# Performance work log

Hardware: AMD Instinct MI355X
Metric: run time of the kernel (lower is better)

## Reference

```python
import jax, jax.numpy as jnp
import numpy as np

HEAD_DIM = 128
N_HEADS = 16
N_KV_HEADS = 4
CHUNK = 256
TOPK = 4
ROPE_THETA = 10000.0


def apply_rope(x, pos):
    # x: [B, S, H, D], NeoX-style (half-split) rotary as in flash-attn RotaryEmbedding
    d = x.shape[-1]
    inv_freq = 1.0 / (ROPE_THETA ** (jnp.arange(0, d, 2, dtype=jnp.float32) / d))  # [D/2]
    ang = pos.astype(jnp.float32)[:, None] * inv_freq[None, :]  # [S, D/2]
    cos = jnp.cos(ang)[None, :, None, :]
    sin = jnp.sin(ang)[None, :, None, :]
    x1, x2 = x[..., : d // 2], x[..., d // 2:]
    return jnp.concatenate([x1 * cos - x2 * sin, x2 * cos + x1 * sin], axis=-1)


def setup_inputs() -> dict:
    key = jax.random.key(0)
    ks = jax.random.split(key, 5)
    B, S, H = 2, 2048, 2048
    hidden_states = jax.random.normal(ks[0], (B, S, H), dtype=jnp.float32)
    wq = jax.random.normal(ks[1], (H, N_HEADS * HEAD_DIM), dtype=jnp.float32) * 0.02
    wk = jax.random.normal(ks[2], (H, N_KV_HEADS * HEAD_DIM), dtype=jnp.float32) * 0.02
    wv = jax.random.normal(ks[3], (H, N_KV_HEADS * HEAD_DIM), dtype=jnp.float32) * 0.02
    wo = jax.random.normal(ks[4], (N_HEADS * HEAD_DIM, H), dtype=jnp.float32) * 0.02
    return {"hidden_states": hidden_states, "wq": wq, "wk": wk, "wv": wv, "wo": wo}


def reference(hidden_states, wq, wk, wv, wo):
    B, S, _ = hidden_states.shape
    q = (hidden_states @ wq).reshape(B, S, N_HEADS, HEAD_DIM)
    k = (hidden_states @ wk).reshape(B, S, N_KV_HEADS, HEAD_DIM)
    v = (hidden_states @ wv).reshape(B, S, N_KV_HEADS, HEAD_DIM)

    pos = jnp.arange(S)
    q = apply_rope(q, pos)
    k = apply_rope(k, pos)

    # GQA: repeat_interleave kv heads to match query heads
    g = N_HEADS // N_KV_HEADS
    k = jnp.repeat(k, g, axis=2)  # [B,S,H,D]
    v = jnp.repeat(v, g, axis=2)

    # ---- MoBA gating: q . mean(K_chunk) ----
    N = S // CHUNK  # number of chunks
    kmean = k.reshape(B, N, CHUNK, N_HEADS, HEAD_DIM).mean(axis=2)  # [B,N,H,D]
    gate = jnp.einsum('bnhd,bshd->bhsn', kmean, q)  # [B,H,S,N]

    chunk_ids = jnp.arange(N)
    chunk_end = (chunk_ids + 1) * CHUNK
    q_chunk = pos // CHUNK
    # chunks not fully before the query are not gate candidates
    gate = jnp.where(pos[None, None, :, None] >= chunk_end[None, None, None, :], gate, -jnp.inf)
    # query's own chunk is always selected
    gate = jnp.where(q_chunk[None, None, :, None] == chunk_ids[None, None, None, :], jnp.inf, gate)

    _, idx = jax.lax.top_k(gate, min(TOPK, N))  # [B,H,S,K]
    sel = jnp.any(idx[..., None] == chunk_ids, axis=-2)  # [B,H,S,N] bool

    # expand chunk selection to per-key mask; combine with causal mask
    allowed = sel[:, :, :, pos // CHUNK]  # [B,H,S,S]
    causal = pos[:, None] >= pos[None, :]  # [S,S]
    mask = allowed & causal[None, None]

    scale = HEAD_DIM ** -0.5
    scores = jnp.einsum('bshd,bthd->bhst', q, k) * scale
    scores = jnp.where(mask, scores, -jnp.inf)
    probs = jax.nn.softmax(scores, axis=-1)
    o = jnp.einsum('bhst,bthd->bshd', probs, v).reshape(B, S, N_HEADS * HEAD_DIM)
    return o @ wo
```

## Files before the change

kernel.cpp:

```cpp
#include <hip/hip_runtime.h>
#include <stdint.h>
#include <math.h>

typedef _Float16 f16x8 __attribute__((ext_vector_type(8)));
typedef float    f32x4 __attribute__((ext_vector_type(4)));
typedef __attribute__((address_space(1))) void as1_void;
typedef __attribute__((address_space(3))) void as3_void;

__device__ __forceinline__ unsigned short f2h(float x) {
    _Float16 h = (_Float16)x;
    return __builtin_bit_cast(unsigned short, h);
}
__device__ __forceinline__ float h2f(unsigned short u) {
    return (float)__builtin_bit_cast(_Float16, u);
}
__device__ __forceinline__ void glds16(const void* g, void* l) {
    __builtin_amdgcn_global_load_lds((as1_void*)g, (as3_void*)l, 16, 0, 0);
}


#define TAU 0.015

__global__ void setup_kernel(float* __restrict__ ct, float* __restrict__ st,
                             double* __restrict__ km, int* __restrict__ flagcnt) {
    int gid = blockIdx.x * 256 + threadIdx.x;
    if (gid == 0) *flagcnt = 0;
    if (gid < 8192) km[gid] = 0.0;
    int i = gid & 63, s = gid >> 6;
    float xf = (float)i * (1.0f / 64.0f);
    float pf = (float)pow(10000.0, (double)xf);
    float inv = 1.0f / pf;
    float ang = (float)s * inv;
    ct[gid] = (float)cos((double)ang);
    st[gid] = (float)sin((double)ang);
}

__global__ __launch_bounds__(256)
void ksum_kernel(const float* __restrict__ hs, const float* __restrict__ ct,
                 const float* __restrict__ st, double* __restrict__ Act,
                 double* __restrict__ Ast) {
    __shared__ float Hs[16][68];
    __shared__ float Tc[16][68];
    __shared__ float Ts[16][68];
    int bn = blockIdx.y;
    int h0 = blockIdx.x * 64;
    int b = bn >> 3, n = bn & 7;
    int t = threadIdx.x;
    int tx = t & 15, ty = t >> 4;
    int d0 = tx * 4, hl0 = ty * 4;
    int si = t & 15, g4 = (t >> 4) * 4;
    double ac[4][4] = {}, as_[4][4] = {};
    for (int s0 = 0; s0 < 256; s0 += 16) {
        __syncthreads();
        int srow = n * 256 + s0 + si;
        *(float4*)&Hs[si][g4] = *(const float4*)&hs[(size_t)(b * 2048 + srow) * 2048 + h0 + g4];
        *(float4*)&Tc[si][g4] = *(const float4*)&ct[srow * 64 + g4];
        *(float4*)&Ts[si][g4] = *(const float4*)&st[srow * 64 + g4];
        __syncthreads();
        #pragma unroll
        for (int kk = 0; kk < 16; ++kk) {
            double hv[4], cv[4], sv[4];
            #pragma unroll
            for (int j = 0; j < 4; ++j) hv[j] = (double)Hs[kk][hl0 + j];
            #pragma unroll
            for (int i = 0; i < 4; ++i) { cv[i] = (double)Tc[kk][d0 + i]; sv[i] = (double)Ts[kk][d0 + i]; }
            #pragma unroll
            for (int i = 0; i < 4; ++i)
                #pragma unroll
                for (int j = 0; j < 4; ++j) {
                    ac[i][j]  = fma(cv[i], hv[j], ac[i][j]);
                    as_[i][j] = fma(sv[i], hv[j], as_[i][j]);
                }
        }
    }
    #pragma unroll
    for (int j = 0; j < 4; ++j) {
        size_t rb = ((size_t)bn * 2048 + h0 + hl0 + j) * 64 + d0;
        double2 c0 = {ac[0][j], ac[1][j]},  c1 = {ac[2][j], ac[3][j]};
        double2 s0_ = {as_[0][j], as_[1][j]}, s1_ = {as_[2][j], as_[3][j]};
        *(double2*)&Act[rb] = c0; *(double2*)&Act[rb + 2] = c1;
        *(double2*)&Ast[rb] = s0_; *(double2*)&Ast[rb + 2] = s1_;
    }
}

__global__ __launch_bounds__(256)
void kmeanw_kernel(const double* __restrict__ Act, const double* __restrict__ Ast,
                   const float* __restrict__ wk, double* __restrict__ km) {
    __shared__ double red[256];
    int blk = blockIdx.x;
    int hp = blk & 3, kvh = (blk >> 2) & 3, bn = blk >> 4;
    int t = threadIdx.x;
    int d = t & 127, sub = t >> 7;
    int jj = d & 63;
    int col1 = kvh * 128 + d;
    int col2 = kvh * 128 + (d ^ 64);
    double sgn = (d < 64) ? -1.0 : 1.0;
    const double* actb = Act + (size_t)bn * 2048 * 64;
    const double* astb = Ast + (size_t)bn * 2048 * 64;
    double acc1 = 0.0, acc2 = 0.0;
    int hbeg = hp * 512 + sub * 256;
    for (int h = hbeg; h < hbeg + 256; ++h) {
        acc1 = fma(actb[(size_t)h * 64 + jj], (double)wk[(size_t)h * 512 + col1], acc1);
        acc2 = fma(astb[(size_t)h * 64 + jj], (double)wk[(size_t)h * 512 + col2], acc2);
    }
    red[t] = acc1 + sgn * acc2;
    __syncthreads();
    if (t < 128) {
        double v = red[t] + red[t + 128];
        atomicAdd(&km[((size_t)bn * 4 + kvh) * 128 + d], v * (1.0 / 256.0));
    }
}

__global__ __launch_bounds__(256)
void ropegate_kernel(float* __restrict__ C, const float* __restrict__ ct,
                     const float* __restrict__ st, const double* __restrict__ km,
                     unsigned int* __restrict__ maskbuf,
                     int* __restrict__ flagcnt, int* __restrict__ flaglist) {
    __shared__ float qbuf[2048];
    int bs = blockIdx.x;
    int s = bs & 2047, b = bs >> 11;
    int t = threadIdx.x;
    size_t base = (size_t)bs * 3072;
    #pragma unroll
    for (int it = 0; it < 5; ++it) {
        int p = t + it * 256;
        int hd = p >> 6, i = p & 63;
        float cs = ct[s * 64 + i], sn = st[s * 64 + i];
        float x1 = C[base + hd * 128 + i];
        float x2 = C[base + hd * 128 + i + 64];
        float n1 = x1 * cs - x2 * sn;
        float n2 = x2 * cs + x1 * sn;
        C[base + hd * 128 + i] = n1;
        C[base + hd * 128 + i + 64] = n2;
        if (hd < 16) { qbuf[hd * 128 + i] = n1; qbuf[hd * 128 + i + 64] = n2; }
    }
    __syncthreads();
    int wave = t >> 6, lane = t & 63;
    int qc = s >> 8;
    const double INF = __builtin_inf();
    #pragma unroll
    for (int ii = 0; ii < 4; ++ii) {
        int h = wave * 4 + ii;
        int kvh = h >> 2;
        double q0 = (double)qbuf[h * 128 + lane];
        double q1 = (double)qbuf[h * 128 + 64 + lane];
        double g[8];
        #pragma unroll
        for (int n = 0; n < 8; ++n) {
            size_t kb = (size_t)((b * 8 + n) * 4 + kvh) * 128;
            double v = q0 * km[kb + lane] + q1 * km[kb + 64 + lane];
            #pragma unroll
            for (int off = 32; off; off >>= 1) v += __shfl_xor(v, off);
            g[n] = v;
        }
        #pragma unroll
        for (int n = 0; n < 8; ++n) {
            if (n == qc)                g[n] = INF;
            else if (s < (n + 1) * 256) g[n] = -INF;
        }
        unsigned int msk = 0;
        for (int p = 0; p < 4; ++p) {
            double best = -INF; int bi = -1;
            #pragma unroll
            for (int n = 0; n < 8; ++n)
                if (!((msk >> n) & 1) && g[n] > best) { best = g[n]; bi = n; }
            if (bi >= 0) msk |= 1u << bi;
        }
        if (lane == 0) {
            int wid = ((b * 16 + h) << 11) + s;
            maskbuf[wid] = msk;
            if (qc >= 4) {
                double worst_in = INF, best_out = -INF;
                #pragma unroll
                for (int n = 0; n < 8; ++n) {
                    if ((msk >> n) & 1) worst_in = fmin(worst_in, g[n]);
                    else if (g[n] > -1e300) best_out = fmax(best_out, g[n]);
                }
                if (worst_in - best_out < TAU) {
                    int ix = atomicAdd(flagcnt, 1);
                    flaglist[ix] = wid;
                }
            }
        }
    }
}

__global__ __launch_bounds__(256)
void repair_kernel(const float* __restrict__ hs, const float* __restrict__ wq,
                   const float* __restrict__ ct, const float* __restrict__ st,
                   const double* __restrict__ km, const int* __restrict__ flagcnt,
                   const int* __restrict__ flaglist, unsigned int* __restrict__ maskbuf) {
    __shared__ double red[256];
    __shared__ double qs[128];
    int nflag = *flagcnt;
    int t = threadIdx.x;
    int d = t & 127, half = t >> 7;
    for (int idx = blockIdx.x; idx < nflag; idx += gridDim.x) {
        int wid = flaglist[idx];
        int s = wid & 2047;
        int h = (wid >> 11) & 15;
        int b = wid >> 15;
        int kvh = h >> 2;
        const float* hrow = hs + (size_t)(b * 2048 + s) * 2048 + half * 1024;
        const float* wcol = wq + (size_t)half * 1024 * 2048 + h * 128 + d;
        double acc = 0.0;
        #pragma unroll 4
        for (int k = 0; k < 1024; ++k)
            acc = fma((double)hrow[k], (double)wcol[(size_t)k * 2048], acc);
        red[t] = acc;
        __syncthreads();
        if (t < 128) qs[t] = red[t] + red[t + 128];
        __syncthreads();
        if (t < 64) {
            double c  = (double)ct[s * 64 + t];
            double sn = (double)st[s * 64 + t];
            double x1 = qs[t], x2 = qs[t + 64];
            qs[t]      = x1 * c - x2 * sn;
            qs[t + 64] = x2 * c + x1 * sn;
        }
        __syncthreads();
        if (t < 64) {
            double g[8];
            #pragma unroll
            for (int n = 0; n < 8; ++n) {
                size_t kb = (size_t)((b * 8 + n) * 4 + kvh) * 128;
                double v = qs[t] * km[kb + t] + qs[t + 64] * km[kb + 64 + t];
                #pragma unroll
                for (int off = 32; off; off >>= 1) v += __shfl_xor(v, off);
                g[n] = v;
            }
            int qc = s >> 8;
            const double INF = __builtin_inf();
            #pragma unroll
            for (int n = 0; n < 8; ++n) {
                if (n == qc)                g[n] = INF;
                else if (s < (n + 1) * 256) g[n] = -INF;
            }
            unsigned int msk = 0;
            for (int p = 0; p < 4; ++p) {
                double best = -INF; int bi = -1;
                #pragma unroll
                for (int n = 0; n < 8; ++n)
                    if (!((msk >> n) & 1) && g[n] > best) { best = g[n]; bi = n; }
                if (bi >= 0) msk |= 1u << bi;
            }
            if (t == 0) maskbuf[wid] = msk;
        }
        __syncthreads();
    }
}


__global__ void split_kernel(const float* __restrict__ src,
                             unsigned short* __restrict__ hi, int n4) {
    int i = blockIdx.x * 256 + threadIdx.x;
    if (i >= n4) return;
    float4 v = ((const float4*)src)[i];
    ushort4 h;
    h.x = f2h(v.x); h.y = f2h(v.y); h.z = f2h(v.z); h.w = f2h(v.w);
    ((ushort4*)hi)[i] = h;
}

__global__ void packall_kernel(const float* __restrict__ wq, const float* __restrict__ wk,
                               const float* __restrict__ wv, const float* __restrict__ wo,
                               unsigned short* __restrict__ Wh, unsigned short* __restrict__ Woh) {
    int gid = blockIdx.x * 256 + threadIdx.x;
    if (gid < 3072 * 512) {
        int n  = gid % 3072;
        int kg = gid / 3072;
        const float* src; int ldn, col;
        if (n < 2048)      { src = wq; ldn = 2048; col = n; }
        else if (n < 2560) { src = wk; ldn = 512;  col = n - 2048; }
        else               { src = wv; ldn = 512;  col = n - 2560; }
        int k0 = kg * 4;
        ushort4 h;
        h.x = f2h(src[(size_t)(k0 + 0) * ldn + col]);
        h.y = f2h(src[(size_t)(k0 + 1) * ldn + col]);
        h.z = f2h(src[(size_t)(k0 + 2) * ldn + col]);
        h.w = f2h(src[(size_t)(k0 + 3) * ldn + col]);
        *(ushort4*)&Wh[(size_t)n * 2048 + k0] = h;
    } else {
        int g2 = gid - 3072 * 512;
        int n  = g2 % 2048;
        int kg = g2 / 2048;
        int k0 = kg * 4;
        ushort4 h;
        h.x = f2h(wo[(size_t)(k0 + 0) * 2048 + n]);
        h.y = f2h(wo[(size_t)(k0 + 1) * 2048 + n]);
        h.z = f2h(wo[(size_t)(k0 + 2) * 2048 + n]);
        h.w = f2h(wo[(size_t)(k0 + 3) * 2048 + n]);
        *(ushort4*)&Woh[(size_t)n * 2048 + k0] = h;
    }
}

__global__ __launch_bounds__(256, 2)
void gemm_kernel(const unsigned short* __restrict__ A_g, const unsigned short* __restrict__ B_g,
                 float* __restrict__ Cg, int M, int N, int K) {
    __shared__ unsigned short Ah[128 * 32];
    __shared__ unsigned short Bh[128 * 32];
    int n0 = blockIdx.x * 128, m0 = blockIdx.y * 128;
    int t = threadIdx.x;
    int wave = t >> 6, lane = t & 63;
    int quad = lane >> 4, l15 = lane & 15;
    int wm = (wave >> 1) * 64, wn = (wave & 1) * 64;

    f32x4 acc[4][4];
    f32x4 zero = {0.f, 0.f, 0.f, 0.f};
    for (int i = 0; i < 4; ++i)
        for (int j = 0; j < 4; ++j) acc[i][j] = zero;

    int srow = lane >> 2, scol = (lane & 3) * 8;
    const unsigned short* Ag0 = &A_g[(size_t)(m0 + wave * 16 + srow) * K + scol];
    const unsigned short* Ag1 = &A_g[(size_t)(m0 + 64 + wave * 16 + srow) * K + scol];
    const unsigned short* Bg0 = &B_g[(size_t)(n0 + wave * 16 + srow) * K + scol];
    const unsigned short* Bg1 = &B_g[(size_t)(n0 + 64 + wave * 16 + srow) * K + scol];
    unsigned short* Al0 = &Ah[(wave * 16) * 32];
    unsigned short* Al1 = &Ah[(64 + wave * 16) * 32];
    unsigned short* Bl0 = &Bh[(wave * 16) * 32];
    unsigned short* Bl1 = &Bh[(64 + wave * 16) * 32];

    for (int k0 = 0; k0 < K; k0 += 32) {
        __syncthreads();
        glds16(Ag0 + k0, Al0);
        glds16(Ag1 + k0, Al1);
        glds16(Bg0 + k0, Bl0);
        glds16(Bg1 + k0, Bl1);
        __syncthreads();
        f16x8 ah[4], bh[4];
        #pragma unroll
        for (int i = 0; i < 4; ++i) {
            ah[i] = *(const f16x8*)&Ah[(wm + i * 16 + l15) * 32 + quad * 8];
            bh[i] = *(const f16x8*)&Bh[(wn + i * 16 + l15) * 32 + quad * 8];
        }
        #pragma unroll
        for (int i = 0; i < 4; ++i)
            #pragma unroll
            for (int j = 0; j < 4; ++j)
                acc[i][j] = __builtin_amdgcn_mfma_f32_16x16x32_f16(ah[i], bh[j], acc[i][j], 0, 0, 0);
    }
    #pragma unroll
    for (int i = 0; i < 4; ++i)
        #pragma unroll
        for (int j = 0; j < 4; ++j)
            #pragma unroll
            for (int r = 0; r < 4; ++r) {
                int row = m0 + wm + i * 16 + quad * 4 + r;
                int col = n0 + wn + j * 16 + l15;
                Cg[(size_t)row * N + col] = acc[i][j][r];
            }
}

__global__ void kvprep_kernel(const float* __restrict__ C, unsigned short* __restrict__ Kh,
                              unsigned short* __restrict__ Vt) {
    __shared__ unsigned short vt[128][72];
    int blk = blockIdx.x;
    int kt = blk & 31, kvh = (blk >> 5) & 3, b = blk >> 7;
    int t = threadIdx.x;
    int key0 = kt * 64;
    #pragma unroll
    for (int it = 0; it < 8; ++it) {
        int idx = t + it * 256;
        int r = idx >> 5, c = (idx & 31) * 4;
        size_t rowb = (size_t)(b * 2048 + key0 + r) * 3072;
        float4 kv = *(const float4*)&C[rowb + 2048 + kvh * 128 + c];
        ushort4 u; u.x = f2h(kv.x); u.y = f2h(kv.y); u.z = f2h(kv.z); u.w = f2h(kv.w);
        *(ushort4*)&Kh[((size_t)(b * 4 + kvh) * 2048 + key0 + r) * 128 + c] = u;
        float4 vv = *(const float4*)&C[rowb + 2560 + kvh * 128 + c];
        vt[c + 0][r] = f2h(vv.x); vt[c + 1][r] = f2h(vv.y);
        vt[c + 2][r] = f2h(vv.z); vt[c + 3][r] = f2h(vv.w);
    }
    __syncthreads();
    #pragma unroll
    for (int it = 0; it < 8; ++it) {
        int idx = t + it * 256;
        int d = idx >> 4, c4 = (idx & 15) * 4;
        *(ushort4*)&Vt[((size_t)(b * 4 + kvh) * 128 + d) * 2048 + key0 + c4] =
            *(ushort4*)&vt[d][c4];
    }
}

__global__ __launch_bounds__(256, 3)
void attn_kernel(const float* __restrict__ C, const unsigned short* __restrict__ Kh,
                 const unsigned short* __restrict__ Vt,
                 const unsigned int* __restrict__ maskbuf,
                 unsigned short* __restrict__ Og) {
    __shared__ unsigned short qv[8704];
    __shared__ unsigned short k_s[8448];
    __shared__ unsigned short p_s[4352];
    __shared__ int kb_list[32];
    __shared__ int nsub_s;
    __shared__ unsigned int umask;

    int bid = blockIdx.x;
    int qt = 31 - (bid >> 5);
    int bh = bid & 31;
    int h = bh & 15, b = bh >> 4;
    int t = threadIdx.x;
    int wave = t >> 6, lane = t & 63;
    int quad = lane >> 4, l15 = lane & 15;
    int w16 = wave * 16;
    int q0 = qt * 64, qc = q0 >> 8, kvh = h >> 2;
    const float NEGINF = -__builtin_inff();

    #pragma unroll
    for (int it = 0; it < 8; ++it) {
        int idx = t + it * 256;
        int r = idx >> 5, c = (idx & 31) * 4;
        float4 v4 = *(const float4*)&C[(size_t)(b * 2048 + q0 + r) * 3072 + h * 128 + c];
        ushort4 u; u.x = f2h(v4.x); u.y = f2h(v4.y); u.z = f2h(v4.z); u.w = f2h(v4.w);
        *(ushort4*)&qv[r * 132 + c] = u;
    }
    if (t == 0) umask = 0;
    int mbase = ((b * 16 + h) << 11) + q0;
    unsigned int am[4];
    #pragma unroll
    for (int r = 0; r < 4; ++r)
        am[r] = maskbuf[mbase + w16 + quad * 4 + r];
    __syncthreads();
    if (t < 64) atomicOr(&umask, maskbuf[mbase + t]);
    f16x8 aq[4];
    #pragma unroll
    for (int ks = 0; ks < 4; ++ks)
        aq[ks] = *(const f16x8*)&qv[(w16 + l15) * 132 + ks * 32 + quad * 8];
    __syncthreads();
    if (t == 0) {
        unsigned int um = umask;
        int n = 0;
        for (int c = 0; c <= qc; ++c) {
            if (!((um >> c) & 1)) continue;
            int submax = (c == qc) ? ((q0 & 255) >> 6) : 3;
            for (int sub = 0; sub <= submax; ++sub) kb_list[n++] = c * 256 + sub * 64;
        }
        nsub_s = n;
    }
    __syncthreads();
    int nsub = nsub_s;

    float m_i[4], l_i[4];
    f32x4 o_acc[8];
    #pragma unroll
    for (int r = 0; r < 4; ++r) { m_i[r] = NEGINF; l_i[r] = 0.f; }
    #pragma unroll
    for (int n = 0; n < 8; ++n) o_acc[n] = (f32x4){0.f, 0.f, 0.f, 0.f};
    const float scale = 0.08838834764831845f;
    const unsigned short* Kb = Kh + (size_t)(b * 4 + kvh) * 2048 * 128;
    const unsigned short* Vb = Vt + (size_t)(b * 4 + kvh) * 128 * 2048;

    int kr = t >> 5, kc = (t & 31) * 4;
    int vr = t >> 4, vc = (t & 15) * 4;

    ushort4 kpre[8], vpre[8];
    {
        int kb0 = kb_list[0];
        #pragma unroll
        for (int it = 0; it < 8; ++it) {
            kpre[it] = *(const ushort4*)&Kb[(size_t)(kb0 + kr + it * 8) * 128 + kc];
            vpre[it] = *(const ushort4*)&Vb[(size_t)(vr + it * 16) * 2048 + kb0 + vc];
        }
    }

    for (int i = 0; i < nsub; ++i) {
        int kbase = kb_list[i];
        __syncthreads();
        #pragma unroll
        for (int it = 0; it < 8; ++it) {
            *(ushort4*)&k_s[(kr + it * 8) * 132 + kc] = kpre[it];
            *(ushort4*)&qv[(vr + it * 16) * 68 + vc] = vpre[it];
        }
        __syncthreads();
        if (i + 1 < nsub) {
            int kbn = kb_list[i + 1];
            #pragma unroll
            for (int it = 0; it < 8; ++it) {
                kpre[it] = *(const ushort4*)&Kb[(size_t)(kbn + kr + it * 8) * 128 + kc];
                vpre[it] = *(const ushort4*)&Vb[(size_t)(vr + it * 16) * 2048 + kbn + vc];
            }
        }
        f32x4 s[4];
        #pragma unroll
        for (int j = 0; j < 4; ++j) {
            f32x4 sj = {0.f, 0.f, 0.f, 0.f};
            #pragma unroll
            for (int ks = 0; ks < 4; ++ks) {
                f16x8 bf = *(const f16x8*)&k_s[(j * 16 + l15) * 132 + ks * 32 + quad * 8];
                sj = __builtin_amdgcn_mfma_f32_16x16x32_f16(aq[ks], bf, sj, 0, 0, 0);
            }
            s[j] = sj;
        }
        #pragma unroll
        for (int r = 0; r < 4; ++r) {
            int qpos = q0 + w16 + quad * 4 + r;
            bool allow = (am[r] >> (kbase >> 8)) & 1;
            float sv[4], rmax = NEGINF;
            #pragma unroll
            for (int j = 0; j < 4; ++j) {
                int kpos = kbase + j * 16 + l15;
                float x = s[j][r] * scale;
                if (!allow || kpos > qpos) x = NEGINF;
                sv[j] = x;
                rmax = fmaxf(rmax, x);
            }
            rmax = fmaxf(rmax, __shfl_xor(rmax, 1));
            rmax = fmaxf(rmax, __shfl_xor(rmax, 2));
            rmax = fmaxf(rmax, __shfl_xor(rmax, 4));
            rmax = fmaxf(rmax, __shfl_xor(rmax, 8));
            float mnew = fmaxf(m_i[r], rmax);
            float alpha = (m_i[r] == NEGINF) ? 0.f : __expf(m_i[r] - mnew);
            float ps[4], lsum = 0.f;
            #pragma unroll
            for (int j = 0; j < 4; ++j) {
                float p = (sv[j] == NEGINF) ? 0.f : __expf(sv[j] - mnew);
                ps[j] = p; lsum += p;
            }
            lsum += __shfl_xor(lsum, 1);
            lsum += __shfl_xor(lsum, 2);
            lsum += __shfl_xor(lsum, 4);
            lsum += __shfl_xor(lsum, 8);
            l_i[r] = l_i[r] * alpha + lsum;
            m_i[r] = mnew;
            #pragma unroll
            for (int n = 0; n < 8; ++n) o_acc[n][r] *= alpha;
            #pragma unroll
            for (int j = 0; j < 4; ++j)
                p_s[(w16 + quad * 4 + r) * 68 + j * 16 + l15] = f2h(ps[j]);
        }
        f16x8 pa0 = *(const f16x8*)&p_s[(w16 + l15) * 68 + quad * 8];
        f16x8 pa1 = *(const f16x8*)&p_s[(w16 + l15) * 68 + 32 + quad * 8];
        #pragma unroll
        for (int n = 0; n < 8; ++n) {
            f16x8 b0 = *(const f16x8*)&qv[(n * 16 + l15) * 68 + quad * 8];
            f16x8 b1 = *(const f16x8*)&qv[(n * 16 + l15) * 68 + 32 + quad * 8];
            o_acc[n] = __builtin_amdgcn_mfma_f32_16x16x32_f16(pa0, b0, o_acc[n], 0, 0, 0);
            o_acc[n] = __builtin_amdgcn_mfma_f32_16x16x32_f16(pa1, b1, o_acc[n], 0, 0, 0);
        }
    }
    __syncthreads();
    #pragma unroll
    for (int r = 0; r < 4; ++r) {
        float inv = (l_i[r] > 0.f) ? 1.f / l_i[r] : 0.f;
        #pragma unroll
        for (int n = 0; n < 8; ++n)
            k_s[(w16 + quad * 4 + r) * 132 + n * 16 + l15] = f2h(o_acc[n][r] * inv);
    }
    __syncthreads();
    #pragma unroll
    for (int it = 0; it < 8; ++it) {
        int idx = t + it * 256;
        int r = idx >> 5, cpos = (idx & 31) * 4;
        *(ushort4*)&Og[(size_t)(b * 2048 + q0 + r) * 2048 + h * 128 + cpos] =
            *(ushort4*)&k_s[r * 132 + cpos];
    }
}

extern "C" void kernel_launch(void* const* d_in, const int* in_sizes, int n_in,
                              void* d_out, int out_size, void* d_ws, size_t ws_size,
                              hipStream_t stream) {
    const float* hs = (const float*)d_in[0];
    const float* wq = (const float*)d_in[1];
    const float* wk = (const float*)d_in[2];
    const float* wv = (const float*)d_in[3];
    const float* wo = (const float*)d_in[4];
    float* out = (float*)d_out;
    char* ws = (char*)d_ws;

    double*         Act  = (double*)       (ws + 37748736);
    double*         Ast  = (double*)       (ws + 54525952);
    unsigned short* hsh  = (unsigned short*)(ws + 0);
    unsigned short* Wth  = (unsigned short*)(ws + 16777216);
    unsigned short* woth = (unsigned short*)(ws + 29360128);
    float*          Cqkv = (float*)        (ws + 37748736);
    unsigned short* Og   = (unsigned short*)(ws + 88080384);
    double*         km64 = (double*)       (ws + 104857600);
    unsigned int*   mskb = (unsigned int*) (ws + 104923136);
    float*          ct   = (float*)        (ws + 105447424);
    float*          st   = (float*)        (ws + 105971712);
    unsigned short* Kh   = (unsigned short*)(ws + 106496000);
    unsigned short* Vt   = (unsigned short*)(ws + 114884608);
    int*            fcnt = (int*)          (ws + 123273216);
    int*            flst = (int*)          (ws + 123273280);

    setup_kernel  <<<512, 256, 0, stream>>>(ct, st, km64, fcnt);
    ksum_kernel   <<<dim3(32, 16), 256, 0, stream>>>(hs, ct, st, Act, Ast);
    kmeanw_kernel <<<256, 256, 0, stream>>>(Act, Ast, wk, km64);
    split_kernel  <<<8192, 256, 0, stream>>>(hs, hsh, 2097152);
    packall_kernel<<<10240, 256, 0, stream>>>(wq, wk, wv, wo, Wth, woth);
    gemm_kernel   <<<dim3(24, 32), 256, 0, stream>>>(hsh, Wth, Cqkv, 4096, 3072, 2048);
    ropegate_kernel<<<4096, 256, 0, stream>>>(Cqkv, ct, st, km64, mskb, fcnt, flst);
    repair_kernel <<<2048, 256, 0, stream>>>(hs, wq, ct, st, km64, fcnt, flst, mskb);
    kvprep_kernel <<<256, 256, 0, stream>>>(Cqkv, Kh, Vt);
    attn_kernel   <<<1024, 256, 0, stream>>>(Cqkv, Kh, Vt, mskb, Og);
    gemm_kernel   <<<dim3(16, 32), 256, 0, stream>>>(Og, woth, out, 4096, 2048, 2048);
}
```

Baseline: 695.7 us.

## Enlarge attention query tile to 128 rows with 512 threads and swizzled K LDS

The attention kernel now processes 128 query rows per block with 8 waves, so each K/V subtile loaded into LDS is shared by twice as many query rows. Q is loaded directly from global into registers, the three separate LDS arrays are merged into one buffer, and the K tile drops its padding in favour of an XOR swizzle to avoid bank conflicts. The GEMM launch bound is also raised to request three blocks per CU. The trade-off is fewer blocks, with some extra masked key subtiles processed for the diagonal chunk, and possible register pressure in the GEMM.

```diff
diff --git a/kernel.cpp b/kernel.cpp
--- a/kernel.cpp
+++ b/kernel.cpp
@@ -293,7 +293,7 @@
     }
 }
 
-__global__ __launch_bounds__(256, 2)
+__global__ __launch_bounds__(256, 3)
 void gemm_kernel(const unsigned short* __restrict__ A_g, const unsigned short* __restrict__ B_g,
                  float* __restrict__ Cg, int M, int N, int K) {
     __shared__ unsigned short Ah[128 * 32];
@@ -379,56 +379,59 @@
     }
 }
 
-__global__ __launch_bounds__(256, 3)
+__global__ __launch_bounds__(512, 4)
 void attn_kernel(const float* __restrict__ C, const unsigned short* __restrict__ Kh,
                  const unsigned short* __restrict__ Vt,
                  const unsigned int* __restrict__ maskbuf,
                  unsigned short* __restrict__ Og) {
-    __shared__ unsigned short qv[8704];
-    __shared__ unsigned short k_s[8448];
-    __shared__ unsigned short p_s[4352];
+    __shared__ unsigned short SH[8704 + 8192 + 8704];
     __shared__ int kb_list[32];
     __shared__ int nsub_s;
     __shared__ unsigned int umask;
+    const int VOFF = 0, KOFF = 8704, POFF = 16896;
 
     int bid = blockIdx.x;
-    int qt = 31 - (bid >> 5);
+    int qt = 15 - (bid >> 5);
     int bh = bid & 31;
     int h = bh & 15, b = bh >> 4;
     int t = threadIdx.x;
     int wave = t >> 6, lane = t & 63;
     int quad = lane >> 4, l15 = lane & 15;
     int w16 = wave * 16;
-    int q0 = qt * 64, qc = q0 >> 8, kvh = h >> 2;
+    int q0 = qt * 128, qc = q0 >> 8, kvh = h >> 2;
     const float NEGINF = -__builtin_inff();
 
-    #pragma unroll
-    for (int it = 0; it < 8; ++it) {
-        int idx = t + it * 256;
-        int r = idx >> 5, c = (idx & 31) * 4;
-        float4 v4 = *(const float4*)&C[(size_t)(b * 2048 + q0 + r) * 3072 + h * 128 + c];
-        ushort4 u; u.x = f2h(v4.x); u.y = f2h(v4.y); u.z = f2h(v4.z); u.w = f2h(v4.w);
-        *(ushort4*)&qv[r * 132 + c] = u;
-    }
+    f16x8 aq[4];
+    {
+        const float* qrow = &C[(size_t)(b * 2048 + q0 + w16 + l15) * 3072 + h * 128];
+        #pragma unroll
+        for (int ks = 0; ks < 4; ++ks) {
+            float4 a  = *(const float4*)&qrow[ks * 32 + quad * 8];
+            float4 c2 = *(const float4*)&qrow[ks * 32 + quad * 8 + 4];
+            f16x8 v;
+            v[0] = (_Float16)a.x;  v[1] = (_Float16)a.y;
+            v[2] = (_Float16)a.z;  v[3] = (_Float16)a.w;
+            v[4] = (_Float16)c2.x; v[5] = (_Float16)c2.y;
+            v[6] = (_Float16)c2.z; v[7] = (_Float16)c2.w;
+            aq[ks] = v;
+        }
+    }
+
     if (t == 0) umask = 0;
+    __syncthreads();
     int mbase = ((b * 16 + h) << 11) + q0;
     unsigned int am[4];
     #pragma unroll
     for (int r = 0; r < 4; ++r)
         am[r] = maskbuf[mbase + w16 + quad * 4 + r];
-    __syncthreads();
-    if (t < 64) atomicOr(&umask, maskbuf[mbase + t]);
-    f16x8 aq[4];
-    #pragma unroll
-    for (int ks = 0; ks < 4; ++ks)
-        aq[ks] = *(const f16x8*)&qv[(w16 + l15) * 132 + ks * 32 + quad * 8];
+    if (t < 128) atomicOr(&umask, maskbuf[mbase + t]);
     __syncthreads();
     if (t == 0) {
         unsigned int um = umask;
         int n = 0;
         for (int c = 0; c <= qc; ++c) {
             if (!((um >> c) & 1)) continue;
-            int submax = (c == qc) ? ((q0 & 255) >> 6) : 3;
+            int submax = (c == qc) ? (((q0 & 255) >> 6) + 1) : 3;
             for (int sub = 0; sub <= submax; ++sub) kb_list[n++] = c * 256 + sub * 64;
         }
         nsub_s = n;
@@ -446,16 +449,16 @@
     const unsigned short* Kb = Kh + (size_t)(b * 4 + kvh) * 2048 * 128;
     const unsigned short* Vb = Vt + (size_t)(b * 4 + kvh) * 128 * 2048;
 
-    int kr = t >> 5, kc = (t & 31) * 4;
-    int vr = t >> 4, vc = (t & 15) * 4;
-
-    ushort4 kpre[8], vpre[8];
+    int krow_s = t >> 5, kcol8 = t & 31;
+    int vrow_s = t >> 4, vcol4 = t & 15;
+
+    ushort4 kpre[4], vpre[4];
     {
         int kb0 = kb_list[0];
         #pragma unroll
-        for (int it = 0; it < 8; ++it) {
-            kpre[it] = *(const ushort4*)&Kb[(size_t)(kb0 + kr + it * 8) * 128 + kc];
-            vpre[it] = *(const ushort4*)&Vb[(size_t)(vr + it * 16) * 2048 + kb0 + vc];
+        for (int it = 0; it < 4; ++it) {
+            kpre[it] = *(const ushort4*)&Kb[(size_t)(kb0 + krow_s + it * 16) * 128 + kcol8 * 4];
+            vpre[it] = *(const ushort4*)&Vb[(size_t)(vrow_s + it * 32) * 2048 + kb0 + vcol4 * 4];
         }
     }
 
@@ -463,26 +466,31 @@
         int kbase = kb_list[i];
         __syncthreads();
         #pragma unroll
-        for (int it = 0; it < 8; ++it) {
-            *(ushort4*)&k_s[(kr + it * 8) * 132 + kc] = kpre[it];
-            *(ushort4*)&qv[(vr + it * 16) * 68 + vc] = vpre[it];
+        for (int it = 0; it < 4; ++it) {
+            int kr = krow_s + it * 16;
+            int kbyte = (kr * 256 + kcol8 * 8) ^ ((kr & 7) << 4);
+            *(ushort4*)&SH[KOFF + (kbyte >> 1)] = kpre[it];
+            *(ushort4*)&SH[VOFF + (vrow_s + it * 32) * 68 + vcol4 * 4] = vpre[it];
         }
         __syncthreads();
         if (i + 1 < nsub) {
             int kbn = kb_list[i + 1];
             #pragma unroll
-            for (int it = 0; it < 8; ++it) {
-                kpre[it] = *(const ushort4*)&Kb[(size_t)(kbn + kr + it * 8) * 128 + kc];
-                vpre[it] = *(const ushort4*)&Vb[(size_t)(vr + it * 16) * 2048 + kbn + vc];
+            for (int it = 0; it < 4; ++it) {
+                kpre[it] = *(const ushort4*)&Kb[(size_t)(kbn + krow_s + it * 16) * 128 + kcol8 * 4];
+                vpre[it] = *(const ushort4*)&Vb[(size_t)(vrow_s + it * 32) * 2048 + kbn + vcol4 * 4];
             }
         }
         f32x4 s[4];
         #pragma unroll
         for (int j = 0; j < 4; ++j) {
             f32x4 sj = {0.f, 0.f, 0.f, 0.f};
+            int krow = j * 16 + l15;
+            int swzb = ((krow & 7) << 4);
             #pragma unroll
             for (int ks = 0; ks < 4; ++ks) {
-                f16x8 bf = *(const f16x8*)&k_s[(j * 16 + l15) * 132 + ks * 32 + quad * 8];
+                int kbyte = (krow * 256 + ks * 64 + quad * 16) ^ swzb;
+                f16x8 bf = *(const f16x8*)&SH[KOFF + (kbyte >> 1)];
                 sj = __builtin_amdgcn_mfma_f32_16x16x32_f16(aq[ks], bf, sj, 0, 0, 0);
             }
             s[j] = sj;
@@ -522,14 +530,14 @@
             for (int n = 0; n < 8; ++n) o_acc[n][r] *= alpha;
             #pragma unroll
             for (int j = 0; j < 4; ++j)
-                p_s[(w16 + quad * 4 + r) * 68 + j * 16 + l15] = f2h(ps[j]);
-        }
-        f16x8 pa0 = *(const f16x8*)&p_s[(w16 + l15) * 68 + quad * 8];
-        f16x8 pa1 = *(const f16x8*)&p_s[(w16 + l15) * 68 + 32 + quad * 8];
+                SH[POFF + (w16 + quad * 4 + r) * 68 + j * 16 + l15] = f2h(ps[j]);
+        }
+        f16x8 pa0 = *(const f16x8*)&SH[POFF + (w16 + l15) * 68 + quad * 8];
+        f16x8 pa1 = *(const f16x8*)&SH[POFF + (w16 + l15) * 68 + 32 + quad * 8];
         #pragma unroll
         for (int n = 0; n < 8; ++n) {
-            f16x8 b0 = *(const f16x8*)&qv[(n * 16 + l15) * 68 + quad * 8];
-            f16x8 b1 = *(const f16x8*)&qv[(n * 16 + l15) * 68 + 32 + quad * 8];
+            f16x8 b0 = *(const f16x8*)&SH[VOFF + (n * 16 + l15) * 68 + quad * 8];
+            f16x8 b1 = *(const f16x8*)&SH[VOFF + (n * 16 + l15) * 68 + 32 + quad * 8];
             o_acc[n] = __builtin_amdgcn_mfma_f32_16x16x32_f16(pa0, b0, o_acc[n], 0, 0, 0);
             o_acc[n] = __builtin_amdgcn_mfma_f32_16x16x32_f16(pa1, b1, o_acc[n], 0, 0, 0);
         }
@@ -540,15 +548,15 @@
         float inv = (l_i[r] > 0.f) ? 1.f / l_i[r] : 0.f;
         #pragma unroll
         for (int n = 0; n < 8; ++n)
-            k_s[(w16 + quad * 4 + r) * 132 + n * 16 + l15] = f2h(o_acc[n][r] * inv);
+            SH[KOFF + (w16 + quad * 4 + r) * 128 + n * 16 + l15] = f2h(o_acc[n][r] * inv);
     }
     __syncthreads();
     #pragma unroll
     for (int it = 0; it < 8; ++it) {
-        int idx = t + it * 256;
-        int r = idx >> 5, cpos = (idx & 31) * 4;
-        *(ushort4*)&Og[(size_t)(b * 2048 + q0 + r) * 2048 + h * 128 + cpos] =
-            *(ushort4*)&k_s[r * 132 + cpos];
+        int idx = t + it * 512;
+        int r = idx >> 5, c4 = (idx & 31) * 4;
+        *(ushort4*)&Og[(size_t)(b * 2048 + q0 + r) * 2048 + h * 128 + c4] =
+            *(ushort4*)&SH[KOFF + r * 128 + c4];
     }
 }
 
@@ -588,6 +596,6 @@
     ropegate_kernel<<<4096, 256, 0, stream>>>(Cqkv, ct, st, km64, mskb, fcnt, flst);
     repair_kernel <<<2048, 256, 0, stream>>>(hs, wq, ct, st, km64, fcnt, flst, mskb);
     kvprep_kernel <<<256, 256, 0, stream>>>(Cqkv, Kh, Vt);
-    attn_kernel   <<<1024, 256, 0, stream>>>(Cqkv, Kh, Vt, mskb, Og);
+    attn_kernel   <<<512, 512, 0, stream>>>(Cqkv, Kh, Vt, mskb, Og);
     gemm_kernel   <<<dim3(16, 32), 256, 0, stream>>>(Og, woth, out, 4096, 2048, 2048);
 }
```

New measurement: 773.7 us. 1.11x slower.
